# Performance work log

Hardware: AMD Instinct MI355X
Metric: run time of the kernel (lower is better)

Reference implementation:

```python
import jax, jax.numpy as jnp
import numpy as np
import math

HEAD_SIZE = 64

def setup_inputs() -> dict:
    key = jax.random.key(0)
    k0, k1, k2, k3 = jax.random.split(key, 4)
    B, T, E, H = 4, 4096, 1024, HEAD_SIZE
    return {
        "x": jax.random.normal(k0, (B, T, E), dtype=jnp.float32),
        "Wq": jax.random.normal(k1, (E, H), dtype=jnp.float32) * (1.0 / math.sqrt(E)),
        "Wk": jax.random.normal(k2, (E, H), dtype=jnp.float32) * (1.0 / math.sqrt(E)),
        "Wv": jax.random.normal(k3, (E, H), dtype=jnp.float32) * (1.0 / math.sqrt(E)),
    }

def reference(x, Wq, Wk, Wv):
    # Single-head attention; faithful to source: softmax FIRST, then divide by sqrt(head_size)
    T = x.shape[-2]
    q = x @ Wq  # [B,T,H]
    k = x @ Wk
    v = x @ Wv
    scores = jnp.einsum('bth,bsh->bts', q, k)  # [B,T,T]
    # 'encoder' mask in this repo = lower-triangular (causal)
    causal = jnp.tril(jnp.ones((T, T), dtype=bool))
    scores = jnp.where(causal, scores, -jnp.inf)
    attn = jax.nn.softmax(scores, axis=-1) / jnp.sqrt(jnp.float32(q.shape[-1]))
    return jnp.einsum('bts,bsh->bth', attn, v)
```

## Files before the change

### kernel.cpp

```cpp
#include <hip/hip_runtime.h>
#include <math.h>

#define BB 4
#define TT 4096
#define EE 1024
#define HH 64

typedef __attribute__((ext_vector_type(8))) short bf16x8;
typedef _Float16 f16x8 __attribute__((ext_vector_type(8)));
typedef __attribute__((ext_vector_type(4))) float f32x4;

#define MFMA16(a, b, c)  __builtin_amdgcn_mfma_f32_16x16x32_bf16(a, b, c, 0, 0, 0)
#define MFMA16F(a, b, c) __builtin_amdgcn_mfma_f32_16x16x32_f16(a, b, c, 0, 0, 0)

__device__ __forceinline__ unsigned short f2bf_rne(float f) {
    unsigned u = __float_as_uint(f);
    unsigned r = u + 0x7fffu + ((u >> 16) & 1u);
    return (unsigned short)(r >> 16);
}
__device__ __forceinline__ float bf2f(unsigned short h) {
    return __uint_as_float(((unsigned)h) << 16);
}
__device__ __forceinline__ unsigned short f2h(float f) {
    union { _Float16 h; unsigned short u; } cv;
    cv.h = (_Float16)f;
    return cv.u;
}

__device__ __forceinline__ void async_copy16(const void* g, void* l) {
    __builtin_amdgcn_global_load_lds(
        (const __attribute__((address_space(1))) void*)g,
        (__attribute__((address_space(3))) void*)l, 16, 0, 0);
}
template<int N>
__device__ __forceinline__ void wait_vm() {
    __builtin_amdgcn_s_waitcnt(0x0f70 | (N & 15) | ((N >> 4) << 14));
}

__global__ __launch_bounds__(256) void wprep_kernel(
    const float* __restrict__ Wq, const float* __restrict__ Wk,
    const float* __restrict__ Wv,
    unsigned short* __restrict__ wt_hi, unsigned short* __restrict__ wt_lo)
{
    __shared__ float ts[64][65];
    const int which = blockIdx.x >> 4;
    const int e0 = (blockIdx.x & 15) * 64;
    const float* W = (which == 0) ? Wq : ((which == 1) ? Wk : Wv);
    const int t = threadIdx.x;
    const int h = t & 63;
    #pragma unroll
    for (int p = 0; p < 16; p++) {
        const int er = (t >> 6) + p * 4;
        ts[er][h] = W[(size_t)(e0 + er) * 64 + h];
    }
    __syncthreads();
    const int ew = t & 63;
    #pragma unroll
    for (int p = 0; p < 16; p++) {
        const int hh = (t >> 6) + p * 4;
        const float f = ts[ew][hh];
        const unsigned short hb = f2bf_rne(f);
        const unsigned short lb = f2bf_rne(f - bf2f(hb));
        const size_t o = (size_t)(which * 64 + hh) * 1024 + e0 + ew;
        wt_hi[o] = hb;
        wt_lo[o] = lb;
    }
}

__global__ __launch_bounds__(512) void proj_kernel(
    const float* __restrict__ x,
    const unsigned short* __restrict__ wt_hi, const unsigned short* __restrict__ wt_lo,
    unsigned short* __restrict__ qhf, unsigned short* __restrict__ qlf,
    unsigned short* __restrict__ kf, unsigned short* __restrict__ vt)
{
    __shared__ __align__(16) unsigned char smem[147456];
    const int tid = threadIdx.x;
    const int w = tid >> 6, lane = tid & 63;
    const int quad = lane >> 4, li = lane & 15;
    const int tg = w & 3, eh = w >> 2;
    const int row0 = (int)blockIdx.x * 64;
    const int tok = row0 + tg * 16 + li;

    f32x4 acc[12];
    #pragma unroll
    for (int mt = 0; mt < 12; mt++) acc[mt] = (f32x4){0.f, 0.f, 0.f, 0.f};

    const float* xr = x + (size_t)tok * EE + eh * 512 + quad * 8;

    const int r_l = lane >> 3, sl = lane & 7;
    const int cg = sl ^ r_l;
    const unsigned short* mat = (cg < 4) ? wt_hi : wt_lo;
    const int ce = (cg & 3) * 8;
    const int sA = (quad ^ (li & 7)) * 8;
    const int sB = ((4 + quad) ^ (li & 7)) * 8;

    auto dma_step = [&](int e0, unsigned char* dstbase) {
        #pragma unroll
        for (int ii = 0; ii < 6; ii++) {
            const int i = w * 6 + ii;
            const int ehc = i / 24;
            const int within = i % 24;
            const int row = within * 8 + r_l;
            const unsigned short* src = mat + (size_t)row * EE + ehc * 512 + e0 + ce;
            async_copy16(src, dstbase + ehc * 24576 + within * 1024);
        }
    };

    dma_step(0, smem);
    float4 fc0 = *(const float4*)(xr + 0);
    float4 fc1 = *(const float4*)(xr + 4);
    dma_step(32, smem + 49152);
    float4 fn0 = *(const float4*)(xr + 32);
    float4 fn1 = *(const float4*)(xr + 36);
    float4 ff0, ff1;

    for (int s = 0; s < 16; s++) {
        const int e0 = s * 32;
        if (s + 2 < 16) {
            dma_step(e0 + 64, smem + ((s + 2) % 3) * 49152);
            ff0 = *(const float4*)(xr + e0 + 64);
            ff1 = *(const float4*)(xr + e0 + 68);
            wait_vm<16>();
        } else if (s + 1 < 16) {
            wait_vm<8>();
        } else {
            wait_vm<0>();
        }
        __builtin_amdgcn_s_barrier();

        float fv[8] = {fc0.x, fc0.y, fc0.z, fc0.w, fc1.x, fc1.y, fc1.z, fc1.w};
        bf16x8 bh, bl;
        #pragma unroll
        for (int jj = 0; jj < 8; jj++) {
            unsigned short hb = f2bf_rne(fv[jj]);
            bh[jj] = (short)hb;
            bl[jj] = (short)f2bf_rne(fv[jj] - bf2f(hb));
        }
        const unsigned short* Wbase =
            (const unsigned short*)(smem + (s % 3) * 49152 + eh * 24576);
        #pragma unroll
        for (int mt = 0; mt < 12; mt++) {
            const unsigned short* rb = Wbase + (mt * 16 + li) * 64;
            bf16x8 Ah = *(const bf16x8*)(rb + sA);
            bf16x8 Al = *(const bf16x8*)(rb + sB);
            acc[mt] = MFMA16(Ah, bh, acc[mt]);
            acc[mt] = MFMA16(Ah, bl, acc[mt]);
            acc[mt] = MFMA16(Al, bh, acc[mt]);
        }
        __builtin_amdgcn_s_barrier();
        fc0 = fn0; fc1 = fn1; fn0 = ff0; fn1 = ff1;
    }

    float* Red = (float*)smem;
    if (eh == 1) {
        #pragma unroll
        for (int mt = 0; mt < 12; mt++)
            #pragma unroll
            for (int r = 0; r < 4; r++)
                Red[(size_t)(tg * 192 + mt * 16 + quad * 4 + r) * 17 + li] = acc[mt][r];
    }
    __syncthreads();
    if (eh == 0) {
        #pragma unroll
        for (int mt = 0; mt < 12; mt++)
            #pragma unroll
            for (int r = 0; r < 4; r++)
                acc[mt][r] += Red[(size_t)(tg * 192 + mt * 16 + quad * 4 + r) * 17 + li];
        const int bb = tok >> 12, tloc = tok & 4095;
        #pragma unroll
        for (int mt = 0; mt < 12; mt++) {
            if (mt < 4) {
                const int h = (mt & 3) * 16 + quad * 4;
                ushort4 hi4, lo4; float f; _Float16 hh;
                union { _Float16 h; unsigned short u; } cv;
                f = acc[mt][0]; hh = (_Float16)f; cv.h = hh; hi4.x = cv.u; lo4.x = f2h(f - (float)hh);
                f = acc[mt][1]; hh = (_Float16)f; cv.h = hh; hi4.y = cv.u; lo4.y = f2h(f - (float)hh);
                f = acc[mt][2]; hh = (_Float16)f; cv.h = hh; hi4.z = cv.u; lo4.z = f2h(f - (float)hh);
                f = acc[mt][3]; hh = (_Float16)f; cv.h = hh; hi4.w = cv.u; lo4.w = f2h(f - (float)hh);
                const size_t o = (size_t)tok * 64 + h;
                *(ushort4*)(qhf + o) = hi4;
                *(ushort4*)(qlf + o) = lo4;
            } else if (mt < 8) {
                const int h = (mt & 3) * 16 + quad * 4;
                ushort4 k4;
                k4.x = f2h(acc[mt][0]); k4.y = f2h(acc[mt][1]);
                k4.z = f2h(acc[mt][2]); k4.w = f2h(acc[mt][3]);
                *(ushort4*)(kf + (size_t)tok * 64 + h) = k4;
            } else {
                const int hv = (mt - 8) * 16 + quad * 4;
                #pragma unroll
                for (int r = 0; r < 4; r++)
                    vt[((size_t)(bb * 64 + hv + r) << 12) + tloc] = f2bf_rne(acc[mt][r]);
            }
        }
    }
}

__global__ __launch_bounds__(512) void flash_kernel(
    const unsigned short* __restrict__ qhf, const unsigned short* __restrict__ qlf,
    const unsigned short* __restrict__ kf,
    const unsigned short* __restrict__ vt, float* __restrict__ out)
{
    __shared__ __align__(16) unsigned char smem[89088];
    const int tid = threadIdx.x;
    const int w = tid >> 6, lane = tid & 63;
    const int quad = lane >> 4, li = lane & 15;
    const int lb = (int)blockIdx.x;
    const int b  = (lb & 7) >> 1;
    const int bx = ((lb >> 3) << 1) | (lb & 1);
    const float SM = 20.0f;

    const _Float16* kb = (const _Float16*)kf + ((size_t)b << 18);
    const unsigned short* vtb = vt + ((size_t)b << 18) + (size_t)li * 4096 + quad * 8;

    unsigned char* kbase = smem + w * 8192;
    unsigned short* PsA = (unsigned short*)(smem + 68608 + w * 2560);
    unsigned short* PsB = PsA + 640;
    float* Op = (float*)smem;
    float* Ml = (float*)(smem + 67584);

    const int r_l8 = lane >> 3, s8 = lane & 7;
    const int slf0 = ((quad)     ^ (li & 7)) * 8;
    const int slf1 = ((4 + quad) ^ (li & 7)) * 8;

    auto dma_tile = [&](int k0, unsigned char* dst) {
        #pragma unroll
        for (int i = 0; i < 4; i++) {
            const int row = i * 8 + r_l8;
            const int c = s8 ^ r_l8;
            async_copy16(kb + (size_t)(k0 + row) * 64 + c * 8, dst + i * 1024);
        }
    };

    #pragma unroll 1
    for (int phase = 0; phase < 2; phase++) {
        const int g = phase ? (127 - bx) : bx;
        const int q0 = g * 32;
        const int n_kt = g + 1;
        const int tok0 = q0 + li, tok1 = tok0 + 16;

        const size_t qo0 = ((size_t)(b << 12) + tok0) * 64 + quad * 8;
        const size_t qo1 = qo0 + 16 * 64;
        const _Float16* qh_p = (const _Float16*)qhf;
        const _Float16* ql_p = (const _Float16*)qlf;
        const f16x8 QhA0 = *(const f16x8*)(qh_p + qo0);
        const f16x8 QhA1 = *(const f16x8*)(qh_p + qo0 + 32);
        const f16x8 QlA0 = *(const f16x8*)(ql_p + qo0);
        const f16x8 QlA1 = *(const f16x8*)(ql_p + qo0 + 32);
        const f16x8 QhB0 = *(const f16x8*)(qh_p + qo1);
        const f16x8 QhB1 = *(const f16x8*)(qh_p + qo1 + 32);
        const f16x8 QlB0 = *(const f16x8*)(ql_p + qo1);
        const f16x8 QlB1 = *(const f16x8*)(ql_p + qo1 + 32);

        f32x4 accA[4], accB[4];
        #pragma unroll
        for (int mt = 0; mt < 4; mt++) {
            accA[mt] = (f32x4){0.f, 0.f, 0.f, 0.f};
            accB[mt] = (f32x4){0.f, 0.f, 0.f, 0.f};
        }
        float lA = 0.f, lB = 0.f;

        bf16x8 Vc[4], Vn[4];
        int bufp = 0;
        if (w < n_kt) {
            dma_tile(w * 32, kbase);
            #pragma unroll
            for (int hf = 0; hf < 4; hf++)
                Vc[hf] = *(const bf16x8*)(vtb + (size_t)hf * 65536 + w * 32);
        }

        for (int kt = w; kt < n_kt; kt += 8) {
            const int k0 = kt * 32;

            if (kt + 8 < n_kt) {
                dma_tile((kt + 8) * 32, kbase + (bufp ^ 1) * 4096);
                #pragma unroll
                for (int hf = 0; hf < 4; hf++)
                    Vn[hf] = *(const bf16x8*)(vtb + (size_t)hf * 65536 + (kt + 8) * 32);
                wait_vm<8>();
            } else {
                wait_vm<0>();
            }
            const _Float16* Kw = (const _Float16*)(kbase + bufp * 4096);

            f32x4 sA[2], sB[2];
            #pragma unroll
            for (int jf = 0; jf < 2; jf++) {
                const _Float16* rb = Kw + (jf * 16 + li) * 64;
                f16x8 K0 = *(const f16x8*)(rb + slf0);
                f16x8 K1 = *(const f16x8*)(rb + slf1);
                f32x4 a = (f32x4){0.f, 0.f, 0.f, 0.f};
                a = MFMA16F(K0, QhA0, a);
                a = MFMA16F(K1, QhA1, a);
                a = MFMA16F(K0, QlA0, a);
                a = MFMA16F(K1, QlA1, a);
                sA[jf] = a;
                f32x4 c2 = (f32x4){0.f, 0.f, 0.f, 0.f};
                c2 = MFMA16F(K0, QhB0, c2);
                c2 = MFMA16F(K1, QhB1, c2);
                c2 = MFMA16F(K0, QlB0, c2);
                c2 = MFMA16F(K1, QlB1, c2);
                sB[jf] = c2;
            }

            if (kt == n_kt - 1) {
                #pragma unroll
                for (int jf = 0; jf < 2; jf++)
                    #pragma unroll
                    for (int r = 0; r < 4; r++) {
                        const int j = k0 + jf * 16 + quad * 4 + r;
                        if (j > tok0) sA[jf][r] = -1e30f;
                        if (j > tok1) sB[jf][r] = -1e30f;
                    }
            }

            #pragma unroll
            for (int jf = 0; jf < 2; jf++)
                #pragma unroll
                for (int r = 0; r < 4; r++) {
                    sA[jf][r] = __expf(sA[jf][r] - SM); lA += sA[jf][r];
                    sB[jf][r] = __expf(sB[jf][r] - SM); lB += sB[jf][r];
                }

            #pragma unroll
            for (int jf = 0; jf < 2; jf++) {
                ushort4 pa, pb;
                pa.x = f2bf_rne(sA[jf][0]); pa.y = f2bf_rne(sA[jf][1]);
                pa.z = f2bf_rne(sA[jf][2]); pa.w = f2bf_rne(sA[jf][3]);
                pb.x = f2bf_rne(sB[jf][0]); pb.y = f2bf_rne(sB[jf][1]);
                pb.z = f2bf_rne(sB[jf][2]); pb.w = f2bf_rne(sB[jf][3]);
                *(ushort4*)&PsA[li * 40 + jf * 16 + quad * 4] = pa;
                *(ushort4*)&PsB[li * 40 + jf * 16 + quad * 4] = pb;
            }
            const bf16x8 PA = *(const bf16x8*)&PsA[li * 40 + quad * 8];
            const bf16x8 PB = *(const bf16x8*)&PsB[li * 40 + quad * 8];

            #pragma unroll
            for (int hf = 0; hf < 4; hf++) {
                accA[hf] = MFMA16(Vc[hf], PA, accA[hf]);
                accB[hf] = MFMA16(Vc[hf], PB, accB[hf]);
            }
            #pragma unroll
            for (int hf = 0; hf < 4; hf++) Vc[hf] = Vn[hf];
            bufp ^= 1;
        }

        lA += __shfl_xor(lA, 16); lA += __shfl_xor(lA, 32);
        lB += __shfl_xor(lB, 16); lB += __shfl_xor(lB, 32);

        __syncthreads();
        #pragma unroll
        for (int mt = 0; mt < 4; mt++)
            #pragma unroll
            for (int r = 0; r < 4; r++) {
                Op[(size_t)w * 2112 + (mt * 16 + quad * 4 + r) * 33 + li]      = accA[mt][r];
                Op[(size_t)w * 2112 + (mt * 16 + quad * 4 + r) * 33 + li + 16] = accB[mt][r];
            }
        if (quad == 0) {
            Ml[w * 32 + li]      = lA;
            Ml[w * 32 + 16 + li] = lB;
        }
        __syncthreads();

        const int i  = tid >> 4;
        const int hc = (tid & 15) * 4;
        float l = 0.f;
        #pragma unroll
        for (int ww = 0; ww < 8; ww++) l += Ml[ww * 32 + i];
        const float inv = 1.0f / (l * 8.0f);
        float4 o = {0.f, 0.f, 0.f, 0.f};
        #pragma unroll
        for (int ww = 0; ww < 8; ww++) {
            const float* base = Op + (size_t)ww * 2112;
            o.x += base[(hc + 0) * 33 + i];
            o.y += base[(hc + 1) * 33 + i];
            o.z += base[(hc + 2) * 33 + i];
            o.w += base[(hc + 3) * 33 + i];
        }
        o.x *= inv; o.y *= inv; o.z *= inv; o.w *= inv;
        *(float4*)(out + ((size_t)(b << 12) + q0 + i) * 64 + hc) = o;
        __syncthreads();
    }
}

extern "C" void kernel_launch(void* const* d_in, const int* in_sizes, int n_in,
                              void* d_out, int out_size, void* d_ws, size_t ws_size,
                              hipStream_t stream)
{
    const float* x  = (const float*)d_in[0];
    const float* Wq = (const float*)d_in[1];
    const float* Wk = (const float*)d_in[2];
    const float* Wv = (const float*)d_in[3];
    float* out = (float*)d_out;

    const size_t n_tok = (size_t)BB * TT * HH;
    unsigned short* qhf = (unsigned short*)d_ws;
    unsigned short* qlf = qhf + n_tok;
    unsigned short* kf  = qlf + n_tok;
    unsigned short* vt  = kf + n_tok;
    unsigned short* wt_hi = vt + n_tok;
    unsigned short* wt_lo = wt_hi + 192 * 1024;

    wprep_kernel<<<48, 256, 0, stream>>>(Wq, Wk, Wv, wt_hi, wt_lo);
    proj_kernel<<<(BB * TT) / 64, 512, 0, stream>>>(x, wt_hi, wt_lo,
                                                    qhf, qlf, kf, vt);
    flash_kernel<<<256, 512, 0, stream>>>(qhf, qlf, kf, vt, out);
}
```

Before: 155.9 us.

## Restructure projection: 32-token blocks split over head columns, fp16 split MFMA

The projection kernel now handles 32 tokens per block, with the 8 waves split across head-output groups instead of across halves of the embedding dimension. This removes the cross-wave reduction through shared memory and cuts LDS use so more blocks fit per CU. Weights and x are split into fp16 hi/lo pairs instead of bf16, so the MFMA path uses f16 instructions. The trade-off is twice as many blocks and a longer reduction loop per block, and fp16 has less range than bf16 for the split terms.

```diff
diff --git a/kernel.cpp b/kernel.cpp
--- a/kernel.cpp
+++ b/kernel.cpp
@@ -59,33 +59,35 @@
     for (int p = 0; p < 16; p++) {
         const int hh = (t >> 6) + p * 4;
         const float f = ts[ew][hh];
-        const unsigned short hb = f2bf_rne(f);
-        const unsigned short lb = f2bf_rne(f - bf2f(hb));
+        union { _Float16 h; unsigned short u; } cv;
+        cv.h = (_Float16)f;
+        const unsigned short hb = cv.u;
+        const unsigned short lb = f2h(f - (float)cv.h);
         const size_t o = (size_t)(which * 64 + hh) * 1024 + e0 + ew;
         wt_hi[o] = hb;
         wt_lo[o] = lb;
     }
 }
 
-__global__ __launch_bounds__(512) void proj_kernel(
+__global__ __launch_bounds__(512, 4) void proj_kernel(
     const float* __restrict__ x,
     const unsigned short* __restrict__ wt_hi, const unsigned short* __restrict__ wt_lo,
     unsigned short* __restrict__ qhf, unsigned short* __restrict__ qlf,
     unsigned short* __restrict__ kf, unsigned short* __restrict__ vt)
 {
-    __shared__ __align__(16) unsigned char smem[147456];
+    __shared__ __align__(16) unsigned char smem[73728];
     const int tid = threadIdx.x;
     const int w = tid >> 6, lane = tid & 63;
     const int quad = lane >> 4, li = lane & 15;
-    const int tg = w & 3, eh = w >> 2;
-    const int row0 = (int)blockIdx.x * 64;
+    const int tg = w & 1, hg = w >> 1;
+    const int row0 = (int)blockIdx.x * 32;
     const int tok = row0 + tg * 16 + li;
 
-    f32x4 acc[12];
+    f32x4 acc[3];
     #pragma unroll
-    for (int mt = 0; mt < 12; mt++) acc[mt] = (f32x4){0.f, 0.f, 0.f, 0.f};
-
-    const float* xr = x + (size_t)tok * EE + eh * 512 + quad * 8;
+    for (int mt = 0; mt < 3; mt++) acc[mt] = (f32x4){0.f, 0.f, 0.f, 0.f};
+
+    const float* xr = x + (size_t)tok * EE + quad * 8;
 
     const int r_l = lane >> 3, sl = lane & 7;
     const int cg = sl ^ r_l;
@@ -96,102 +98,84 @@
 
     auto dma_step = [&](int e0, unsigned char* dstbase) {
         #pragma unroll
-        for (int ii = 0; ii < 6; ii++) {
-            const int i = w * 6 + ii;
-            const int ehc = i / 24;
-            const int within = i % 24;
-            const int row = within * 8 + r_l;
-            const unsigned short* src = mat + (size_t)row * EE + ehc * 512 + e0 + ce;
-            async_copy16(src, dstbase + ehc * 24576 + within * 1024);
+        for (int ii = 0; ii < 3; ii++) {
+            const int i = w * 3 + ii;
+            const int row = i * 8 + r_l;
+            const unsigned short* src = mat + (size_t)row * EE + e0 + ce;
+            async_copy16(src, dstbase + i * 1024);
         }
     };
 
     dma_step(0, smem);
     float4 fc0 = *(const float4*)(xr + 0);
     float4 fc1 = *(const float4*)(xr + 4);
-    dma_step(32, smem + 49152);
+    dma_step(32, smem + 24576);
     float4 fn0 = *(const float4*)(xr + 32);
     float4 fn1 = *(const float4*)(xr + 36);
     float4 ff0, ff1;
 
-    for (int s = 0; s < 16; s++) {
+    for (int s = 0; s < 32; s++) {
         const int e0 = s * 32;
-        if (s + 2 < 16) {
-            dma_step(e0 + 64, smem + ((s + 2) % 3) * 49152);
+        if (s + 2 < 32) {
+            dma_step(e0 + 64, smem + ((s + 2) % 3) * 24576);
             ff0 = *(const float4*)(xr + e0 + 64);
             ff1 = *(const float4*)(xr + e0 + 68);
-            wait_vm<16>();
-        } else if (s + 1 < 16) {
-            wait_vm<8>();
+            wait_vm<10>();
+        } else if (s + 1 < 32) {
+            wait_vm<5>();
         } else {
             wait_vm<0>();
         }
         __builtin_amdgcn_s_barrier();
 
         float fv[8] = {fc0.x, fc0.y, fc0.z, fc0.w, fc1.x, fc1.y, fc1.z, fc1.w};
-        bf16x8 bh, bl;
+        f16x8 bh, bl;
         #pragma unroll
         for (int jj = 0; jj < 8; jj++) {
-            unsigned short hb = f2bf_rne(fv[jj]);
-            bh[jj] = (short)hb;
-            bl[jj] = (short)f2bf_rne(fv[jj] - bf2f(hb));
-        }
-        const unsigned short* Wbase =
-            (const unsigned short*)(smem + (s % 3) * 49152 + eh * 24576);
-        #pragma unroll
-        for (int mt = 0; mt < 12; mt++) {
-            const unsigned short* rb = Wbase + (mt * 16 + li) * 64;
-            bf16x8 Ah = *(const bf16x8*)(rb + sA);
-            bf16x8 Al = *(const bf16x8*)(rb + sB);
-            acc[mt] = MFMA16(Ah, bh, acc[mt]);
-            acc[mt] = MFMA16(Ah, bl, acc[mt]);
-            acc[mt] = MFMA16(Al, bh, acc[mt]);
+            const _Float16 hh = (_Float16)fv[jj];
+            bh[jj] = hh;
+            bl[jj] = (_Float16)(fv[jj] - (float)hh);
+        }
+        const _Float16* Wbase = (const _Float16*)(smem + (s % 3) * 24576);
+        #pragma unroll
+        for (int mt = 0; mt < 3; mt++) {
+            const _Float16* rb = Wbase + (size_t)(hg * 48 + mt * 16 + li) * 64;
+            f16x8 Ah = *(const f16x8*)(rb + sA);
+            f16x8 Al = *(const f16x8*)(rb + sB);
+            acc[mt] = MFMA16F(Ah, bh, acc[mt]);
+            acc[mt] = MFMA16F(Ah, bl, acc[mt]);
+            acc[mt] = MFMA16F(Al, bh, acc[mt]);
         }
         __builtin_amdgcn_s_barrier();
         fc0 = fn0; fc1 = fn1; fn0 = ff0; fn1 = ff1;
     }
 
-    float* Red = (float*)smem;
-    if (eh == 1) {
-        #pragma unroll
-        for (int mt = 0; mt < 12; mt++)
+    const int bb = tok >> 12, tloc = tok & 4095;
+    #pragma unroll
+    for (int mt = 0; mt < 3; mt++) {
+        const int h192 = hg * 48 + mt * 16;
+        if (h192 < 64) {
+            const int h = h192 + quad * 4;
+            ushort4 hi4, lo4; float f; _Float16 hh;
+            union { _Float16 h; unsigned short u; } cv;
+            f = acc[mt][0]; hh = (_Float16)f; cv.h = hh; hi4.x = cv.u; lo4.x = f2h(f - (float)hh);
+            f = acc[mt][1]; hh = (_Float16)f; cv.h = hh; hi4.y = cv.u; lo4.y = f2h(f - (float)hh);
+            f = acc[mt][2]; hh = (_Float16)f; cv.h = hh; hi4.z = cv.u; lo4.z = f2h(f - (float)hh);
+            f = acc[mt][3]; hh = (_Float16)f; cv.h = hh; hi4.w = cv.u; lo4.w = f2h(f - (float)hh);
+            const size_t o = (size_t)tok * 64 + h;
+            *(ushort4*)(qhf + o) = hi4;
+            *(ushort4*)(qlf + o) = lo4;
+        } else if (h192 < 128) {
+            const int h = h192 - 64 + quad * 4;
+            ushort4 k4;
+            k4.x = f2h(acc[mt][0]); k4.y = f2h(acc[mt][1]);
+            k4.z = f2h(acc[mt][2]); k4.w = f2h(acc[mt][3]);
+            *(ushort4*)(kf + (size_t)tok * 64 + h) = k4;
+        } else {
+            const int hv = h192 - 128 + quad * 4;
             #pragma unroll
             for (int r = 0; r < 4; r++)
-                Red[(size_t)(tg * 192 + mt * 16 + quad * 4 + r) * 17 + li] = acc[mt][r];
-    }
-    __syncthreads();
-    if (eh == 0) {
-        #pragma unroll
-        for (int mt = 0; mt < 12; mt++)
-            #pragma unroll
-            for (int r = 0; r < 4; r++)
-                acc[mt][r] += Red[(size_t)(tg * 192 + mt * 16 + quad * 4 + r) * 17 + li];
-        const int bb = tok >> 12, tloc = tok & 4095;
-        #pragma unroll
-        for (int mt = 0; mt < 12; mt++) {
-            if (mt < 4) {
-                const int h = (mt & 3) * 16 + quad * 4;
-                ushort4 hi4, lo4; float f; _Float16 hh;
-                union { _Float16 h; unsigned short u; } cv;
-                f = acc[mt][0]; hh = (_Float16)f; cv.h = hh; hi4.x = cv.u; lo4.x = f2h(f - (float)hh);
-                f = acc[mt][1]; hh = (_Float16)f; cv.h = hh; hi4.y = cv.u; lo4.y = f2h(f - (float)hh);
-                f = acc[mt][2]; hh = (_Float16)f; cv.h = hh; hi4.z = cv.u; lo4.z = f2h(f - (float)hh);
-                f = acc[mt][3]; hh = (_Float16)f; cv.h = hh; hi4.w = cv.u; lo4.w = f2h(f - (float)hh);
-                const size_t o = (size_t)tok * 64 + h;
-                *(ushort4*)(qhf + o) = hi4;
-                *(ushort4*)(qlf + o) = lo4;
-            } else if (mt < 8) {
-                const int h = (mt & 3) * 16 + quad * 4;
-                ushort4 k4;
-                k4.x = f2h(acc[mt][0]); k4.y = f2h(acc[mt][1]);
-                k4.z = f2h(acc[mt][2]); k4.w = f2h(acc[mt][3]);
-                *(ushort4*)(kf + (size_t)tok * 64 + h) = k4;
-            } else {
-                const int hv = (mt - 8) * 16 + quad * 4;
-                #pragma unroll
-                for (int r = 0; r < 4; r++)
-                    vt[((size_t)(bb * 64 + hv + r) << 12) + tloc] = f2bf_rne(acc[mt][r]);
-            }
+                vt[((size_t)(bb * 64 + hv + r) << 12) + tloc] = f2bf_rne(acc[mt][r]);
         }
     }
 }
@@ -402,7 +386,7 @@
     unsigned short* wt_lo = wt_hi + 192 * 1024;
 
     wprep_kernel<<<48, 256, 0, stream>>>(Wq, Wk, Wv, wt_hi, wt_lo);
-    proj_kernel<<<(BB * TT) / 64, 512, 0, stream>>>(x, wt_hi, wt_lo,
+    proj_kernel<<<(BB * TT) / 32, 512, 0, stream>>>(x, wt_hi, wt_lo,
                                                     qhf, qlf, kf, vt);
     flash_kernel<<<256, 512, 0, stream>>>(qhf, qlf, kf, vt, out);
 }
```

New measurement: 175.1 us. +12.3%, slower.
